# Kernel tuning notes

Measured on AMD Instinct MI355X. Metric: run time of the kernel, lower is better.

Reference implementation:

```python
import jax, jax.numpy as jnp
import numpy as np

D_MODEL = 512
NHEAD = 8


def setup_inputs() -> dict:
    key = jax.random.key(0)
    k0, k1, k2 = jax.random.split(key, 3)
    s = 1.0 / np.sqrt(D_MODEL)  # torch default uniform init bound (xavier-ish)
    return {
        "x": jax.random.normal(k0, (2, 4096, D_MODEL), dtype=jnp.float32),
        "in_proj_w": jax.random.uniform(k1, (3 * D_MODEL, D_MODEL), jnp.float32, -s, s),
        "in_proj_b": jnp.zeros((3 * D_MODEL,), jnp.float32),
        "out_proj_w": jax.random.uniform(k2, (D_MODEL, D_MODEL), jnp.float32, -s, s),
        "out_proj_b": jnp.zeros((D_MODEL,), jnp.float32),
        "window_size": 128,
    }


def reference(x, in_proj_w, in_proj_b, out_proj_w, out_proj_b, window_size):
    # Faithful to nn.MultiheadAttention (eval mode, dropout inactive).
    # NOTE: PyTorch bool attn_mask: True = disallowed. The module sets True
    # INSIDE the window, so in-window positions are masked OUT.
    B, S, D = x.shape
    H = NHEAD
    hd = D // H

    qkv = x @ in_proj_w.T + in_proj_b                      # [B,S,3D]
    q, k, v = jnp.split(qkv, 3, axis=-1)
    q = q.reshape(B, S, H, hd).transpose(0, 2, 1, 3)       # [B,H,S,hd]
    k = k.reshape(B, S, H, hd).transpose(0, 2, 1, 3)
    v = v.reshape(B, S, H, hd).transpose(0, 2, 1, 3)

    scores = jnp.einsum('bhqd,bhkd->bhqk', q, k) / jnp.sqrt(jnp.float32(hd))

    idx = jnp.arange(S)
    in_window = jnp.abs(idx[:, None] - idx[None, :]) <= window_size  # [S,S]
    scores = jnp.where(in_window, -jnp.inf, scores)

    attn = jax.nn.softmax(scores, axis=-1)                 # [B,H,S,S]
    ctx = jnp.einsum('bhqk,bhkd->bhqd', attn, v)           # [B,H,S,hd]
    ctx = ctx.transpose(0, 2, 1, 3).reshape(B, S, D)       # [B,S,D]
    return ctx @ out_proj_w.T + out_proj_b
```

## Files before the change

kernel.cpp:

```cpp
#include <hip/hip_runtime.h>
#include <hip/hip_bf16.h>

typedef unsigned short u16;
typedef __bf16 bf16x8 __attribute__((ext_vector_type(8)));
typedef short s16x4 __attribute__((ext_vector_type(4)));
typedef float f32x4 __attribute__((ext_vector_type(4)));

__device__ __forceinline__ f32x4 mfma16(bf16x8 a, bf16x8 b, f32x4 c) {
    return __builtin_amdgcn_mfma_f32_16x16x32_bf16(a, b, c, 0, 0, 0);
}
__device__ __forceinline__ f32x4 mfma16k16(s16x4 a, s16x4 b, f32x4 c) {
    return __builtin_amdgcn_mfma_f32_16x16x16bf16_1k(a, b, c, 0, 0, 0);
}

__device__ __forceinline__ u16 f2b(float x) {
    union { float f; unsigned u; } a; a.f = x;
    unsigned r = a.u + 0x7fffu + ((a.u >> 16) & 1u);
    return (u16)(r >> 16);
}
__device__ __forceinline__ unsigned f2b2(float a, float b) {
    union { __hip_bfloat162 h; unsigned u; } cv;
    cv.h = __float22bfloat162_rn(make_float2(a, b));
    return cv.u;
}
__device__ __forceinline__ void async16(const u16* g, u16* l) {
    __builtin_amdgcn_global_load_lds((const __attribute__((address_space(1))) unsigned int*)g,
                                     (__attribute__((address_space(3))) unsigned int*)l, 16, 0, 0);
}

#define NX  (8192 * 512)
#define NWQ (1536 * 512)
#define NWO (512 * 512)
__global__ __launch_bounds__(256) void k_cast_all(const float* __restrict__ x,
                                                  const float* __restrict__ wq,
                                                  const float* __restrict__ wo,
                                                  u16* __restrict__ xb,
                                                  u16* __restrict__ wqb,
                                                  u16* __restrict__ wob) {
    int i = (blockIdx.x * 256 + threadIdx.x) * 4;
    const float* s; u16* d; int off;
    if (i < NX)            { s = x;  d = xb;  off = i; }
    else if (i < NX + NWQ) { s = wq; d = wqb; off = i - NX; }
    else                   { s = wo; d = wob; off = i - NX - NWQ; }
    float4 f = *(const float4*)&s[off];
    uint2 o = make_uint2(f2b2(f.x, f.y), f2b2(f.z, f.w));
    *(uint2*)&d[off] = o;
}

__global__ __launch_bounds__(256, 3) void k_gemm_qkv(const u16* __restrict__ xb,
                                                     const u16* __restrict__ wb,
                                                     const float* __restrict__ bias,
                                                     u16* __restrict__ qkvout) {
    __shared__ u16 AL[2][4096];
    __shared__ u16 WL[2][4096];
    const int tid = threadIdx.x;
    const int w = tid >> 6, lane = tid & 63, l15 = lane & 15, quad = lane >> 4;
    const int mb = blockIdx.x * 128, nb = blockIdx.y * 128;

    f32x4 acc[2][8];
#pragma unroll
    for (int i = 0; i < 2; i++)
#pragma unroll
        for (int j = 0; j < 8; j++) acc[i][j] = (f32x4){0.f, 0.f, 0.f, 0.f};

    const u16* agp = xb + (size_t)(mb + w * 32 + (lane >> 2)) * 512 + (lane & 3) * 8;
    const u16* wgp = wb + (size_t)(nb + w * 32 + (lane >> 2)) * 512 + (lane & 3) * 8;
    const int ldst = w * 1024 + lane * 8;

    async16(agp, &AL[0][ldst]);
    async16(agp + 16 * 512, &AL[0][ldst + 512]);
    async16(wgp, &WL[0][ldst]);
    async16(wgp + 16 * 512, &WL[0][ldst + 512]);
    __syncthreads();
    int p = 0;
    for (int ks = 0; ks < 16; ks++) {
        if (ks < 15) {
            int k0n = (ks + 1) * 32;
            async16(agp + k0n, &AL[p ^ 1][ldst]);
            async16(agp + 16 * 512 + k0n, &AL[p ^ 1][ldst + 512]);
            async16(wgp + k0n, &WL[p ^ 1][ldst]);
            async16(wgp + 16 * 512 + k0n, &WL[p ^ 1][ldst + 512]);
        }
        bf16x8 a0 = *(const bf16x8*)&AL[p][(w * 32 + l15) * 32 + quad * 8];
        bf16x8 a1 = *(const bf16x8*)&AL[p][(w * 32 + 16 + l15) * 32 + quad * 8];
#pragma unroll
        for (int nt = 0; nt < 8; nt++) {
            bf16x8 bfr = *(const bf16x8*)&WL[p][(nt * 16 + l15) * 32 + quad * 8];
            acc[0][nt] = mfma16(a0, bfr, acc[0][nt]);
            acc[1][nt] = mfma16(a1, bfr, acc[1][nt]);
        }
        if (ks < 15) { __syncthreads(); p ^= 1; }
    }
    const int seg = nb >> 9;
    u16* obase = qkvout + (size_t)seg * (16ull * 4096 * 64);
    if (seg < 2) {
        const float sc = (seg == 0) ? 0.125f * 1.44269504088896340736f : 1.0f;
#pragma unroll
        for (int mt = 0; mt < 2; mt++)
#pragma unroll
            for (int nt = 0; nt < 8; nt++) {
                int dcol = nb + nt * 16 + l15;
                int hh = (dcol >> 6) & 7, dloc = dcol & 63;
                float bs = bias[dcol];
#pragma unroll
                for (int r = 0; r < 4; r++) {
                    int m = mb + w * 32 + mt * 16 + quad * 4 + r;
                    float vv = (acc[mt][nt][r] + bs) * sc;
                    int b = m >> 12, s = m & 4095;
                    obase[((size_t)((b * 8 + hh) * 4096 + s)) * 64 + dloc] = f2b(vv);
                }
            }
    } else {
#pragma unroll
        for (int mt = 0; mt < 2; mt++)
#pragma unroll
            for (int nt = 0; nt < 8; nt++) {
                int c = nb + nt * 16 + l15;
                int hh = (c >> 6) & 7, d = c & 63;
                int mbv = d >> 4, l15v = d & 15;
                float bs = bias[c];
                int m0 = mb + w * 32 + mt * 16 + quad * 4;
                int b = m0 >> 12, si = m0 & 4095;
                int kt = si >> 6, ka = si & 63;
                int ntv = ka >> 4;
                uint2 o = make_uint2(f2b2(acc[mt][nt][0] + bs, acc[mt][nt][1] + bs),
                                     f2b2(acc[mt][nt][2] + bs, acc[mt][nt][3] + bs));
                size_t F4 = ((((((size_t)(b * 8 + hh) * 64 + kt) * 4 + ntv) * 4 + mbv) * 4 + quad) * 16 + l15v);
                *(uint2*)&obase[F4 * 4] = o;
            }
    }
}

__global__ __launch_bounds__(128, 2) void k_attn(const u16* __restrict__ qg,
                                                 const u16* __restrict__ kg,
                                                 const u16* __restrict__ vfg,
                                                 u16* __restrict__ ctx,
                                                 const int* __restrict__ win) {
    __shared__ u16 KL[2][4096];
    __shared__ u16 VL[2][4096];
    const int tid = threadIdx.x;
    const int w = tid >> 6, lane = tid & 63, l15 = lane & 15, quad = lane >> 4;
    const int bh = blockIdx.y;
    const int qb0 = blockIdx.x * 64;
    const int qb0w = qb0 + w * 32;
    const int W = win[0];
    const size_t bhb = (size_t)bh * 4096 * 64;

    bf16x8 qf[2][2];
#pragma unroll
    for (int g = 0; g < 2; g++) {
        const u16* qrow = &qg[bhb + (size_t)(qb0w + g * 16 + l15) * 64];
        qf[g][0] = *(const bf16x8*)&qrow[quad * 8];
        qf[g][1] = *(const bf16x8*)&qrow[32 + quad * 8];
    }
    s16x4 onesA;
    {
        short v = (l15 == 0) ? (short)0x3F80 : (short)0;
        onesA[0] = v; onesA[1] = v; onesA[2] = v; onesA[3] = v;
    }

    f32x4 O[2][4];
#pragma unroll
    for (int g = 0; g < 2; g++)
#pragma unroll
        for (int mb = 0; mb < 4; mb++) O[g][mb] = (f32x4){0.f, 0.f, 0.f, 0.f};
    f32x4 O1[2] = {(f32x4){0.f, 0.f, 0.f, 0.f}, (f32x4){0.f, 0.f, 0.f, 0.f}};

    const u16* kgp = kg + bhb + (size_t)(w * 32 + (lane >> 3)) * 64
                     + (((lane & 7) ^ (lane >> 3)) * 8);
    const u16* vgp = vfg + bhb + (size_t)(w * 2048 + lane * 8);
    const int ldst = w * 2048 + lane * 8;

    auto skip = [&](int kb) { return max(qb0 + 63 - kb, kb + 63 - qb0) <= W; };
    int kb = 0;
    while (kb < 4096 && skip(kb)) kb += 64;
    {
        const u16* kt_p = kgp + (size_t)kb * 64;
        const u16* vt_p = vgp + (size_t)(kb >> 6) * 4096;
#pragma unroll
        for (int t = 0; t < 4; t++) async16(kt_p + t * 512, &KL[0][ldst + t * 512]);
#pragma unroll
        for (int t = 0; t < 4; t++) async16(vt_p + t * 512, &VL[0][ldst + t * 512]);
    }
    __syncthreads();
    int p = 0;
    while (kb < 4096) {
        int kb_next = kb + 64;
        while (kb_next < 4096 && skip(kb_next)) kb_next += 64;
        if (kb_next < 4096) {
            const u16* kt_p = kgp + (size_t)kb_next * 64;
            const u16* vt_p = vgp + (size_t)(kb_next >> 6) * 4096;
#pragma unroll
            for (int t = 0; t < 4; t++) async16(kt_p + t * 512, &KL[p ^ 1][ldst + t * 512]);
#pragma unroll
            for (int t = 0; t < 4; t++) async16(vt_p + t * 512, &VL[p ^ 1][ldst + t * 512]);
        }
        const bool partial = (kb + 63 >= qb0 - W) && (kb <= qb0 + 63 + W);
        bf16x8 kf[4][2];
        const int rs = l15 & 7;
#pragma unroll
        for (int nt = 0; nt < 4; nt++) {
            kf[nt][0] = *(const bf16x8*)&KL[p][(nt * 16 + l15) * 64 + ((quad ^ rs) * 8)];
            kf[nt][1] = *(const bf16x8*)&KL[p][(nt * 16 + l15) * 64 + (((quad + 4) ^ rs) * 8)];
        }
        s16x4 vfr[16];
#pragma unroll
        for (int f = 0; f < 16; f++)
            vfr[f] = *(const s16x4*)&VL[p][((f * 4 + quad) * 16 + l15) * 4];

        f32x4 C[2][4];
#pragma unroll
        for (int g = 0; g < 2; g++)
#pragma unroll
            for (int nt = 0; nt < 4; nt++) {
                f32x4 z = (f32x4){0.f, 0.f, 0.f, 0.f};
                C[g][nt] = mfma16(kf[nt][0], qf[g][0], z);
                C[g][nt] = mfma16(kf[nt][1], qf[g][1], C[g][nt]);
            }
        s16x4 pb[2][4];
        if (!partial) {
#pragma unroll
            for (int g = 0; g < 2; g++)
#pragma unroll
                for (int nt = 0; nt < 4; nt++) {
                    float p0 = __builtin_amdgcn_exp2f(C[g][nt][0]);
                    float p1 = __builtin_amdgcn_exp2f(C[g][nt][1]);
                    float p2 = __builtin_amdgcn_exp2f(C[g][nt][2]);
                    float p3 = __builtin_amdgcn_exp2f(C[g][nt][3]);
                    union { uint2 u; s16x4 v; } pk;
                    pk.u = make_uint2(f2b2(p0, p1), f2b2(p2, p3));
                    pb[g][nt] = pk.v;
                }
        } else {
#pragma unroll
            for (int g = 0; g < 2; g++) {
                int qr = qb0w + g * 16 + l15;
#pragma unroll
                for (int nt = 0; nt < 4; nt++) {
                    float pv[4];
#pragma unroll
                    for (int r = 0; r < 4; r++) {
                        int key = kb + nt * 16 + quad * 4 + r;
                        int dd = qr - key; dd = dd < 0 ? -dd : dd;
                        pv[r] = (dd <= W) ? 0.f : __builtin_amdgcn_exp2f(C[g][nt][r]);
                    }
                    union { uint2 u; s16x4 v; } pk;
                    pk.u = make_uint2(f2b2(pv[0], pv[1]), f2b2(pv[2], pv[3]));
                    pb[g][nt] = pk.v;
                }
            }
        }
#pragma unroll
        for (int nt = 0; nt < 4; nt++)
#pragma unroll
            for (int g = 0; g < 2; g++) {
#pragma unroll
                for (int mb = 0; mb < 4; mb++)
                    O[g][mb] = mfma16k16(vfr[nt * 4 + mb], pb[g][nt], O[g][mb]);
                O1[g] = mfma16k16(onesA, pb[g][nt], O1[g]);
            }
        if (kb_next < 4096) { __syncthreads(); p ^= 1; }
        kb = kb_next;
    }
    int b = bh >> 3, h = bh & 7;
#pragma unroll
    for (int g = 0; g < 2; g++) {
        float ls = __shfl(O1[g][0], l15);
        float inv = 1.0f / ls;
        int qr = qb0w + g * 16 + l15;
        size_t rowoff = ((size_t)(b * 4096 + qr)) * 512 + h * 64;
#pragma unroll
        for (int mb = 0; mb < 4; mb++) {
            uint2 o = make_uint2(f2b2(O[g][mb][0] * inv, O[g][mb][1] * inv),
                                 f2b2(O[g][mb][2] * inv, O[g][mb][3] * inv));
            *(uint2*)&ctx[rowoff + mb * 16 + quad * 4] = o;
        }
    }
}

__global__ __launch_bounds__(256, 2) void k_gemm_out(const u16* __restrict__ ab,
                                                     const u16* __restrict__ wb,
                                                     const float* __restrict__ bias,
                                                     float* __restrict__ out) {
    __shared__ u16 AL[2][4096];
    __shared__ u16 WL[2][2048];
    const int tid = threadIdx.x;
    const int w = tid >> 6, lane = tid & 63, l15 = lane & 15, quad = lane >> 4;
    const int mb = blockIdx.x * 128, nb = blockIdx.y * 64;

    f32x4 acc[2][4];
#pragma unroll
    for (int i = 0; i < 2; i++)
#pragma unroll
        for (int j = 0; j < 4; j++) acc[i][j] = (f32x4){0.f, 0.f, 0.f, 0.f};

    const u16* agp = ab + (size_t)(mb + w * 32 + (lane >> 2)) * 512 + (lane & 3) * 8;
    const u16* wgp = wb + (size_t)(nb + w * 16 + (lane >> 2)) * 512 + (lane & 3) * 8;
    const int ldstA = w * 1024 + lane * 8;
    const int ldstW = w * 512 + lane * 8;

    async16(agp, &AL[0][ldstA]);
    async16(agp + 16 * 512, &AL[0][ldstA + 512]);
    async16(wgp, &WL[0][ldstW]);
    __syncthreads();
    int p = 0;
    for (int ks = 0; ks < 16; ks++) {
        if (ks < 15) {
            int k0n = (ks + 1) * 32;
            async16(agp + k0n, &AL[p ^ 1][ldstA]);
            async16(agp + 16 * 512 + k0n, &AL[p ^ 1][ldstA + 512]);
            async16(wgp + k0n, &WL[p ^ 1][ldstW]);
        }
        bf16x8 a0 = *(const bf16x8*)&AL[p][(w * 32 + l15) * 32 + quad * 8];
        bf16x8 a1 = *(const bf16x8*)&AL[p][(w * 32 + 16 + l15) * 32 + quad * 8];
#pragma unroll
        for (int nt = 0; nt < 4; nt++) {
            bf16x8 bfr = *(const bf16x8*)&WL[p][(nt * 16 + l15) * 32 + quad * 8];
            acc[0][nt] = mfma16(a0, bfr, acc[0][nt]);
            acc[1][nt] = mfma16(a1, bfr, acc[1][nt]);
        }
        if (ks < 15) { __syncthreads(); p ^= 1; }
    }
#pragma unroll
    for (int mt = 0; mt < 2; mt++)
#pragma unroll
        for (int nt = 0; nt < 4; nt++) {
            int n = nb + nt * 16 + l15;
            float bs = bias[n];
#pragma unroll
            for (int r = 0; r < 4; r++) {
                int m = mb + w * 32 + mt * 16 + quad * 4 + r;
                out[(size_t)m * 512 + n] = acc[mt][nt][r] + bs;
            }
        }
}

extern "C" void kernel_launch(void* const* d_in, const int* in_sizes, int n_in,
                              void* d_out, int out_size, void* d_ws, size_t ws_size,
                              hipStream_t stream) {
    const float* x    = (const float*)d_in[0];
    const float* wqkv = (const float*)d_in[1];
    const float* bqkv = (const float*)d_in[2];
    const float* wout = (const float*)d_in[3];
    const float* bout = (const float*)d_in[4];
    const int*   win  = (const int*)d_in[5];
    float* out = (float*)d_out;

    u16* xb    = (u16*)d_ws;
    u16* wqkvb = xb    + 8192ull * 512;
    u16* woutb = wqkvb + 1536ull * 512;
    u16* qkvb  = woutb + 512ull * 512;
    u16* ctxb  = qkvb  + 3ull * 16 * 4096 * 64;

    k_cast_all<<<5120, 256, 0, stream>>>(x, wqkv, wout, xb, wqkvb, woutb);
    k_gemm_qkv<<<dim3(64, 12), 256, 0, stream>>>(xb, wqkvb, bqkv, qkvb);
    k_attn<<<dim3(64, 16), 128, 0, stream>>>(qkvb, qkvb + 16ull * 4096 * 64,
                                             qkvb + 32ull * 4096 * 64, ctxb, win);
    k_gemm_out<<<dim3(64, 8), 256, 0, stream>>>(ctxb, woutb, bout, out);
}
```

Before: 213.6 us.

## Use K=32 bf16 MFMA for PV, pre-swizzle K/V layouts, widen attention blocks

The QKV GEMM epilogue now writes K and V in fragment-ready layouts, so the attention kernel can load K/V tiles with plain contiguous async copies and feed the 16x16x32 bf16 MFMA for both QK^T and PV instead of the older 16x16x16 instruction. The attention block grows to 4 waves covering 128 query rows, which halves the number of K/V tile loads per query. In exchange the K store in the GEMM epilogue becomes scalar 2-byte writes, and each block skips fewer fully masked key tiles because its query span is wider.

```diff
diff --git a/kernel.cpp b/kernel.cpp
--- a/kernel.cpp
+++ b/kernel.cpp
@@ -3,14 +3,10 @@
 
 typedef unsigned short u16;
 typedef __bf16 bf16x8 __attribute__((ext_vector_type(8)));
-typedef short s16x4 __attribute__((ext_vector_type(4)));
 typedef float f32x4 __attribute__((ext_vector_type(4)));
 
 __device__ __forceinline__ f32x4 mfma16(bf16x8 a, bf16x8 b, f32x4 c) {
     return __builtin_amdgcn_mfma_f32_16x16x32_bf16(a, b, c, 0, 0, 0);
-}
-__device__ __forceinline__ f32x4 mfma16k16(s16x4 a, s16x4 b, f32x4 c) {
-    return __builtin_amdgcn_mfma_f32_16x16x16bf16_1k(a, b, c, 0, 0, 0);
 }
 
 __device__ __forceinline__ u16 f2b(float x) {
@@ -93,8 +89,8 @@
     }
     const int seg = nb >> 9;
     u16* obase = qkvout + (size_t)seg * (16ull * 4096 * 64);
-    if (seg < 2) {
-        const float sc = (seg == 0) ? 0.125f * 1.44269504088896340736f : 1.0f;
+    if (seg == 0) {
+        const float sc = 0.125f * 1.44269504088896340736f;
 #pragma unroll
         for (int mt = 0; mt < 2; mt++)
 #pragma unroll
@@ -109,6 +105,25 @@
                     int b = m >> 12, s = m & 4095;
                     obase[((size_t)((b * 8 + hh) * 4096 + s)) * 64 + dloc] = f2b(vv);
                 }
+            }
+    } else if (seg == 1) {
+#pragma unroll
+        for (int mt = 0; mt < 2; mt++)
+#pragma unroll
+            for (int nt = 0; nt < 8; nt++) {
+                int dcol = nb + nt * 16 + l15;
+                int hh = (dcol >> 6) & 7, d = dcol & 63;
+                int h2 = d >> 5, qk = (d >> 3) & 3, j = d & 7;
+                float bs = bias[dcol];
+                int m0 = mb + w * 32 + mt * 16 + quad * 4;
+                int b = m0 >> 12, s0 = m0 & 4095;
+                int kt = s0 >> 6, ksx = s0 & 63;
+                int kg2 = ksx >> 5, rem = ksx & 31;
+                int t2 = (rem >> 2) & 1, lb = (rem >> 3) * 4;
+                size_t base = ((((((size_t)(b * 8 + hh) * 64 + kt) * 2 + kg2) * 2 + t2) * 2 + h2) * 4 + qk) * 16 + lb;
+#pragma unroll
+                for (int r = 0; r < 4; r++)
+                    obase[(base + r) * 8 + j] = f2b(acc[mt][nt][r] + bs);
             }
     } else {
 #pragma unroll
@@ -121,18 +136,18 @@
                 float bs = bias[c];
                 int m0 = mb + w * 32 + mt * 16 + quad * 4;
                 int b = m0 >> 12, si = m0 & 4095;
-                int kt = si >> 6, ka = si & 63;
-                int ntv = ka >> 4;
+                int kt = si >> 6, ksx = si & 63;
+                int kg2 = ksx >> 5, qv = (ksx >> 3) & 3, j0 = ksx & 7;
                 uint2 o = make_uint2(f2b2(acc[mt][nt][0] + bs, acc[mt][nt][1] + bs),
                                      f2b2(acc[mt][nt][2] + bs, acc[mt][nt][3] + bs));
-                size_t F4 = ((((((size_t)(b * 8 + hh) * 64 + kt) * 4 + ntv) * 4 + mbv) * 4 + quad) * 16 + l15v);
-                *(uint2*)&obase[F4 * 4] = o;
-            }
-    }
-}
-
-__global__ __launch_bounds__(128, 2) void k_attn(const u16* __restrict__ qg,
-                                                 const u16* __restrict__ kg,
+                size_t F = (((((size_t)(b * 8 + hh) * 64 + kt) * 2 + kg2) * 4 + mbv) * 4 + qv) * 16 + l15v;
+                *(uint2*)&obase[F * 8 + j0] = o;
+            }
+    }
+}
+
+__global__ __launch_bounds__(256, 2) void k_attn(const u16* __restrict__ qg,
+                                                 const u16* __restrict__ kfg,
                                                  const u16* __restrict__ vfg,
                                                  u16* __restrict__ ctx,
                                                  const int* __restrict__ win) {
@@ -141,7 +156,7 @@
     const int tid = threadIdx.x;
     const int w = tid >> 6, lane = tid & 63, l15 = lane & 15, quad = lane >> 4;
     const int bh = blockIdx.y;
-    const int qb0 = blockIdx.x * 64;
+    const int qb0 = blockIdx.x * 128;
     const int qb0w = qb0 + w * 32;
     const int W = win[0];
     const size_t bhb = (size_t)bh * 4096 * 64;
@@ -153,10 +168,13 @@
         qf[g][0] = *(const bf16x8*)&qrow[quad * 8];
         qf[g][1] = *(const bf16x8*)&qrow[32 + quad * 8];
     }
-    s16x4 onesA;
+    bf16x8 ones8;
     {
-        short v = (l15 == 0) ? (short)0x3F80 : (short)0;
-        onesA[0] = v; onesA[1] = v; onesA[2] = v; onesA[3] = v;
+        u16 v = (l15 == 0) ? (u16)0x3F80 : (u16)0;
+        union { u16 a[8]; bf16x8 b; } c;
+#pragma unroll
+        for (int i = 0; i < 8; i++) c.a[i] = v;
+        ones8 = c.b;
     }
 
     f32x4 O[2][4];
@@ -166,21 +184,20 @@
         for (int mb = 0; mb < 4; mb++) O[g][mb] = (f32x4){0.f, 0.f, 0.f, 0.f};
     f32x4 O1[2] = {(f32x4){0.f, 0.f, 0.f, 0.f}, (f32x4){0.f, 0.f, 0.f, 0.f}};
 
-    const u16* kgp = kg + bhb + (size_t)(w * 32 + (lane >> 3)) * 64
-                     + (((lane & 7) ^ (lane >> 3)) * 8);
-    const u16* vgp = vfg + bhb + (size_t)(w * 2048 + lane * 8);
-    const int ldst = w * 2048 + lane * 8;
-
-    auto skip = [&](int kb) { return max(qb0 + 63 - kb, kb + 63 - qb0) <= W; };
+    const u16* kbase = kfg + bhb;
+    const u16* vbase = vfg + bhb;
+    const int soff = w * 1024 + lane * 8;
+
+    auto skip = [&](int kb) { return max(qb0 + 127 - kb, kb + 63 - qb0) <= W; };
     int kb = 0;
     while (kb < 4096 && skip(kb)) kb += 64;
     {
-        const u16* kt_p = kgp + (size_t)kb * 64;
-        const u16* vt_p = vgp + (size_t)(kb >> 6) * 4096;
-#pragma unroll
-        for (int t = 0; t < 4; t++) async16(kt_p + t * 512, &KL[0][ldst + t * 512]);
-#pragma unroll
-        for (int t = 0; t < 4; t++) async16(vt_p + t * 512, &VL[0][ldst + t * 512]);
+        const u16* kt_p = kbase + (size_t)(kb >> 6) * 4096;
+        const u16* vt_p = vbase + (size_t)(kb >> 6) * 4096;
+        async16(kt_p + soff, &KL[0][soff]);
+        async16(kt_p + soff + 512, &KL[0][soff + 512]);
+        async16(vt_p + soff, &VL[0][soff]);
+        async16(vt_p + soff + 512, &VL[0][soff + 512]);
     }
     __syncthreads();
     int p = 0;
@@ -188,76 +205,89 @@
         int kb_next = kb + 64;
         while (kb_next < 4096 && skip(kb_next)) kb_next += 64;
         if (kb_next < 4096) {
-            const u16* kt_p = kgp + (size_t)kb_next * 64;
-            const u16* vt_p = vgp + (size_t)(kb_next >> 6) * 4096;
-#pragma unroll
-            for (int t = 0; t < 4; t++) async16(kt_p + t * 512, &KL[p ^ 1][ldst + t * 512]);
-#pragma unroll
-            for (int t = 0; t < 4; t++) async16(vt_p + t * 512, &VL[p ^ 1][ldst + t * 512]);
-        }
-        const bool partial = (kb + 63 >= qb0 - W) && (kb <= qb0 + 63 + W);
-        bf16x8 kf[4][2];
-        const int rs = l15 & 7;
-#pragma unroll
-        for (int nt = 0; nt < 4; nt++) {
-            kf[nt][0] = *(const bf16x8*)&KL[p][(nt * 16 + l15) * 64 + ((quad ^ rs) * 8)];
-            kf[nt][1] = *(const bf16x8*)&KL[p][(nt * 16 + l15) * 64 + (((quad + 4) ^ rs) * 8)];
-        }
-        s16x4 vfr[16];
-#pragma unroll
-        for (int f = 0; f < 16; f++)
-            vfr[f] = *(const s16x4*)&VL[p][((f * 4 + quad) * 16 + l15) * 4];
-
-        f32x4 C[2][4];
+            const u16* kt_p = kbase + (size_t)(kb_next >> 6) * 4096;
+            const u16* vt_p = vbase + (size_t)(kb_next >> 6) * 4096;
+            async16(kt_p + soff, &KL[p ^ 1][soff]);
+            async16(kt_p + soff + 512, &KL[p ^ 1][soff + 512]);
+            async16(vt_p + soff, &VL[p ^ 1][soff]);
+            async16(vt_p + soff + 512, &VL[p ^ 1][soff + 512]);
+        }
+        const bool partial = (kb + 63 >= qb0 - W) && (kb <= qb0 + 127 + W);
+        bf16x8 kf[2][2][2];
+#pragma unroll
+        for (int kg = 0; kg < 2; kg++)
+#pragma unroll
+            for (int t = 0; t < 2; t++)
+#pragma unroll
+                for (int h = 0; h < 2; h++)
+                    kf[kg][t][h] = *(const bf16x8*)&KL[p][((((kg * 2 + t) * 2 + h) * 4 + quad) * 16 + l15) * 8];
+        bf16x8 vfr[2][4];
+#pragma unroll
+        for (int kg = 0; kg < 2; kg++)
+#pragma unroll
+            for (int mb = 0; mb < 4; mb++)
+                vfr[kg][mb] = *(const bf16x8*)&VL[p][(((kg * 4 + mb) * 4 + quad) * 16 + l15) * 8];
+
+        f32x4 C[2][2][2];
 #pragma unroll
         for (int g = 0; g < 2; g++)
 #pragma unroll
-            for (int nt = 0; nt < 4; nt++) {
-                f32x4 z = (f32x4){0.f, 0.f, 0.f, 0.f};
-                C[g][nt] = mfma16(kf[nt][0], qf[g][0], z);
-                C[g][nt] = mfma16(kf[nt][1], qf[g][1], C[g][nt]);
-            }
-        s16x4 pb[2][4];
+            for (int kg = 0; kg < 2; kg++)
+#pragma unroll
+                for (int t = 0; t < 2; t++) {
+                    f32x4 z = (f32x4){0.f, 0.f, 0.f, 0.f};
+                    C[g][kg][t] = mfma16(kf[kg][t][0], qf[g][0], z);
+                    C[g][kg][t] = mfma16(kf[kg][t][1], qf[g][1], C[g][kg][t]);
+                }
+        bf16x8 pb[2][2];
         if (!partial) {
 #pragma unroll
             for (int g = 0; g < 2; g++)
 #pragma unroll
-                for (int nt = 0; nt < 4; nt++) {
-                    float p0 = __builtin_amdgcn_exp2f(C[g][nt][0]);
-                    float p1 = __builtin_amdgcn_exp2f(C[g][nt][1]);
-                    float p2 = __builtin_amdgcn_exp2f(C[g][nt][2]);
-                    float p3 = __builtin_amdgcn_exp2f(C[g][nt][3]);
-                    union { uint2 u; s16x4 v; } pk;
-                    pk.u = make_uint2(f2b2(p0, p1), f2b2(p2, p3));
-                    pb[g][nt] = pk.v;
+                for (int kg = 0; kg < 2; kg++) {
+                    float p0 = __builtin_amdgcn_exp2f(C[g][kg][0][0]);
+                    float p1 = __builtin_amdgcn_exp2f(C[g][kg][0][1]);
+                    float p2 = __builtin_amdgcn_exp2f(C[g][kg][0][2]);
+                    float p3 = __builtin_amdgcn_exp2f(C[g][kg][0][3]);
+                    float p4 = __builtin_amdgcn_exp2f(C[g][kg][1][0]);
+                    float p5 = __builtin_amdgcn_exp2f(C[g][kg][1][1]);
+                    float p6 = __builtin_amdgcn_exp2f(C[g][kg][1][2]);
+                    float p7 = __builtin_amdgcn_exp2f(C[g][kg][1][3]);
+                    union { uint4 u; bf16x8 v; } pk;
+                    pk.u = make_uint4(f2b2(p0, p1), f2b2(p2, p3), f2b2(p4, p5), f2b2(p6, p7));
+                    pb[g][kg] = pk.v;
                 }
         } else {
 #pragma unroll
             for (int g = 0; g < 2; g++) {
                 int qr = qb0w + g * 16 + l15;
 #pragma unroll
-                for (int nt = 0; nt < 4; nt++) {
-                    float pv[4];
-#pragma unroll
-                    for (int r = 0; r < 4; r++) {
-                        int key = kb + nt * 16 + quad * 4 + r;
-                        int dd = qr - key; dd = dd < 0 ? -dd : dd;
-                        pv[r] = (dd <= W) ? 0.f : __builtin_amdgcn_exp2f(C[g][nt][r]);
-                    }
-                    union { uint2 u; s16x4 v; } pk;
-                    pk.u = make_uint2(f2b2(pv[0], pv[1]), f2b2(pv[2], pv[3]));
-                    pb[g][nt] = pk.v;
+                for (int kg = 0; kg < 2; kg++) {
+                    float pv[8];
+#pragma unroll
+                    for (int t = 0; t < 2; t++)
+#pragma unroll
+                        for (int r = 0; r < 4; r++) {
+                            int key = kb + kg * 32 + 8 * quad + 4 * t + r;
+                            int dd = qr - key; dd = dd < 0 ? -dd : dd;
+                            pv[t * 4 + r] = (dd <= W) ? 0.f
+                                          : __builtin_amdgcn_exp2f(C[g][kg][t][r]);
+                        }
+                    union { uint4 u; bf16x8 v; } pk;
+                    pk.u = make_uint4(f2b2(pv[0], pv[1]), f2b2(pv[2], pv[3]),
+                                      f2b2(pv[4], pv[5]), f2b2(pv[6], pv[7]));
+                    pb[g][kg] = pk.v;
                 }
             }
         }
 #pragma unroll
-        for (int nt = 0; nt < 4; nt++)
+        for (int kg = 0; kg < 2; kg++)
 #pragma unroll
             for (int g = 0; g < 2; g++) {
 #pragma unroll
                 for (int mb = 0; mb < 4; mb++)
-                    O[g][mb] = mfma16k16(vfr[nt * 4 + mb], pb[g][nt], O[g][mb]);
-                O1[g] = mfma16k16(onesA, pb[g][nt], O1[g]);
+                    O[g][mb] = mfma16(vfr[kg][mb], pb[g][kg], O[g][mb]);
+                O1[g] = mfma16(ones8, pb[g][kg], O1[g]);
             }
         if (kb_next < 4096) { __syncthreads(); p ^= 1; }
         kb = kb_next;
@@ -354,7 +384,7 @@
 
     k_cast_all<<<5120, 256, 0, stream>>>(x, wqkv, wout, xb, wqkvb, woutb);
     k_gemm_qkv<<<dim3(64, 12), 256, 0, stream>>>(xb, wqkvb, bqkv, qkvb);
-    k_attn<<<dim3(64, 16), 128, 0, stream>>>(qkvb, qkvb + 16ull * 4096 * 64,
+    k_attn<<<dim3(32, 16), 256, 0, stream>>>(qkvb, qkvb + 16ull * 4096 * 64,
                                              qkvb + 32ull * 4096 * 64, ctxb, win);
     k_gemm_out<<<dim3(64, 8), 256, 0, stream>>>(ctxb, woutb, bout, out);
 }
```

Result: faster. 198.7 us (-7.0%).
